# Kernel tuning notes

Hardware: AMD Instinct MI355X
Metric: run time of the kernel (lower is better)

Reference implementation:

```python
import jax, jax.numpy as jnp
import numpy as np
import math

EMBED = 512
KDIM = 512
VDIM = 512
H = 8
HD = EMBED // H
N = 2048
L = 2048
B = 4


def setup_inputs() -> dict:
    key = jax.random.key(0)
    ks = jax.random.split(key, 14)
    s = 1.0 / math.sqrt(EMBED)
    return {
        "q": jax.random.normal(ks[0], (N, B, EMBED), jnp.float32),
        "k": jax.random.normal(ks[1], (L, B, KDIM), jnp.float32),
        "v": jax.random.normal(ks[2], (L, B, VDIM), jnp.float32),
        "pe1": jax.random.normal(ks[3], (B, N, 3), jnp.float32),
        "pe2": jax.random.normal(ks[4], (L, 3), jnp.float32),
        "Wq": jax.random.normal(ks[5], (EMBED, EMBED), jnp.float32) * s,
        "bq": jnp.zeros((EMBED,), jnp.float32),
        "Wk": jax.random.normal(ks[6], (EMBED, KDIM), jnp.float32) * s,
        "bk": jnp.zeros((EMBED,), jnp.float32),
        "Wv": jax.random.normal(ks[7], (EMBED, VDIM), jnp.float32) * s,
        "bv": jnp.zeros((EMBED,), jnp.float32),
        "Wo": jax.random.normal(ks[8], (EMBED, EMBED), jnp.float32) * s,
        "bo": jnp.zeros((EMBED,), jnp.float32),
    }


def reference(q, k, v, pe1, pe2, Wq, bq, Wk, bk, Wv, bv, Wo, bo):
    n, b, _ = q.shape
    l = k.shape[0]
    # projections (nn.Linear: x @ W.T + b)
    qp = q @ Wq.T + bq  # (n, b, E)
    kp = k @ Wk.T + bk  # (l, b, E)
    vp = v @ Wv.T + bv  # (l, b, E)
    # split heads -> (b, H, n, hd)
    qh = qp.reshape(n, b, H, HD).transpose(1, 2, 0, 3)
    kh = kp.reshape(l, b, H, HD).transpose(1, 2, 0, 3)
    vh = vp.reshape(l, b, H, HD).transpose(1, 2, 0, 3)
    # relative PE bias: (b, n, l), broadcast over heads
    pe_scores = jnp.einsum('bnc,lc->bnl', pe1, pe2)[:, None, :, :]
    scores = (jnp.einsum('bhnd,bhld->bhnl', qh, kh) + pe_scores) / math.sqrt(HD)
    attn = jax.nn.softmax(scores, axis=-1)
    out = jnp.einsum('bhnl,bhld->bhnd', attn, vh)  # (b, H, n, hd)
    out = out.transpose(2, 0, 1, 3).reshape(n, b, EMBED)
    return out @ Wo.T + bo
```

## Files before the change

### kernel.cpp

```cpp
#include <hip/hip_runtime.h>
#include <math.h>

#define EMBED 512
#define HDIM 64
#define NHEADS 8
#define SEQ_N 2048
#define SEQ_L 2048
#define BATCH 4
#define MROWS (SEQ_N*BATCH)
#define BE (BATCH*EMBED)

#define QSCALE 0.18033688f

typedef _Float16 f16;
typedef _Float16 half8 __attribute__((ext_vector_type(8)));
typedef _Float16 half4 __attribute__((ext_vector_type(4)));
typedef _Float16 half2v __attribute__((ext_vector_type(2)));
typedef float floatx4 __attribute__((ext_vector_type(4)));
typedef float floatx16 __attribute__((ext_vector_type(16)));

static __device__ inline float fast_exp2(float x) {
#if __has_builtin(__builtin_amdgcn_exp2f)
  return __builtin_amdgcn_exp2f(x);
#else
  return __expf(x * 0.69314718056f);
#endif
}

static __device__ inline half2v pk2(float a, float b) {
#if __has_builtin(__builtin_amdgcn_cvt_pkrtz)
  return __builtin_bit_cast(half2v, __builtin_amdgcn_cvt_pkrtz(a, b));
#else
  half2v o; o[0] = (f16)a; o[1] = (f16)b; return o;
#endif
}

static __device__ inline void gload16(const void* g, void* l) {
  __builtin_amdgcn_global_load_lds(
      (__attribute__((address_space(1))) void*)(g),
      (__attribute__((address_space(3))) void*)(l), 16, 0, 0);
}

__global__ __launch_bounds__(256) void cvt_all(const float* __restrict__ q,
                                               const float* __restrict__ k,
                                               const float* __restrict__ v,
                                               const float* __restrict__ Wq,
                                               const float* __restrict__ Wk,
                                               const float* __restrict__ Wv,
                                               const float* __restrict__ Wo,
                                               f16* __restrict__ qb, f16* __restrict__ kb,
                                               f16* __restrict__ vb, f16* __restrict__ Wb) {
  const long TOK = (long)MROWS * EMBED;
  const long WSZ = (long)EMBED * EMBED;
  int y = blockIdx.y;
  long i = ((long)blockIdx.x * 256 + threadIdx.x) * 4;
  if (y < 3) {
    if (i < TOK) {
      const float* s = y == 0 ? q : y == 1 ? k : v;
      f16* d = y == 0 ? qb : y == 1 ? kb : vb;
      float4 f = *reinterpret_cast<const float4*>(s + i);
      half4 o; o[0] = (f16)f.x; o[1] = (f16)f.y; o[2] = (f16)f.z; o[3] = (f16)f.w;
      *reinterpret_cast<half4*>(d + i) = o;
    }
  } else {
    if (i < 4 * WSZ) {
      int sel = (int)(i >> 18);
      long off = i & (WSZ - 1);
      const float* s = sel == 0 ? Wq : sel == 1 ? Wk : sel == 2 ? Wv : Wo;
      float4 f = *reinterpret_cast<const float4*>(s + off);
      half4 o; o[0] = (f16)f.x; o[1] = (f16)f.y; o[2] = (f16)f.z; o[3] = (f16)f.w;
      *reinterpret_cast<half4*>(Wb + i) = o;
    }
  }
}

__global__ __launch_bounds__(256) void gemm_qkv(const f16* __restrict__ A0,
                                                const f16* __restrict__ A1,
                                                const f16* __restrict__ A2,
                                                const f16* __restrict__ W0,
                                                const f16* __restrict__ W1,
                                                const f16* __restrict__ W2,
                                                const float* __restrict__ b0,
                                                const float* __restrict__ b1,
                                                const float* __restrict__ b2,
                                                f16* __restrict__ C0, f16* __restrict__ C1,
                                                f16* __restrict__ C2) {
  __shared__ alignas(16) f16 As[2][128 * 32];
  __shared__ alignas(16) f16 Bs[2][128 * 32];
  const int sel = blockIdx.y >> 2;
  const f16* A = sel == 0 ? A0 : sel == 1 ? A1 : A2;
  const f16* Bt = sel == 0 ? W0 : sel == 1 ? W1 : W2;
  const float* bias = sel == 0 ? b0 : sel == 1 ? b1 : b2;
  const float scl = sel == 0 ? QSCALE : 1.0f;
  f16* C = sel == 0 ? C0 : sel == 1 ? C1 : C2;
  const int tid = threadIdx.x;
  const int wave = tid >> 6, lane = tid & 63, quad = lane >> 4, l16 = lane & 15;
  const int wm = wave & 1, wn = wave >> 1;
  const long m0 = (long)blockIdx.x * 128;
  const long n0 = (long)(blockIdx.y & 3) * 128;
  const int srow = lane >> 2;
  const int scol = (lane & 3) * 8;

  const f16* Ag0 = A + (m0 + wave * 32 + srow) * EMBED + scol;
  const f16* Ag1 = A + (m0 + wave * 32 + 16 + srow) * EMBED + scol;
  const f16* Bg0 = Bt + (n0 + wave * 32 + srow) * EMBED + scol;
  const f16* Bg1 = Bt + (n0 + wave * 32 + 16 + srow) * EMBED + scol;

  gload16(Ag0, &As[0][(wave * 32) * 32]);
  gload16(Ag1, &As[0][(wave * 32 + 16) * 32]);
  gload16(Bg0, &Bs[0][(wave * 32) * 32]);
  gload16(Bg1, &Bs[0][(wave * 32 + 16) * 32]);
  floatx4 acc[4][4] = {};
  asm volatile("s_waitcnt vmcnt(0)" ::: "memory");
  __builtin_amdgcn_s_barrier();

#pragma unroll
  for (int ks = 0; ks < 16; ++ks) {
    const int cur = ks & 1;
    if (ks + 1 < 16) {
      const int k1 = (ks + 1) * 32;
      gload16(Ag0 + k1, &As[cur ^ 1][(wave * 32) * 32]);
      gload16(Ag1 + k1, &As[cur ^ 1][(wave * 32 + 16) * 32]);
      gload16(Bg0 + k1, &Bs[cur ^ 1][(wave * 32) * 32]);
      gload16(Bg1 + k1, &Bs[cur ^ 1][(wave * 32 + 16) * 32]);
    }
    half8 af[4], bf[4];
#pragma unroll
    for (int i = 0; i < 4; ++i)
      af[i] = *reinterpret_cast<const half8*>(&As[cur][(wm * 64 + i * 16 + l16) * 32 + quad * 8]);
#pragma unroll
    for (int j = 0; j < 4; ++j)
      bf[j] = *reinterpret_cast<const half8*>(&Bs[cur][(wn * 64 + j * 16 + l16) * 32 + quad * 8]);
#pragma unroll
    for (int i = 0; i < 4; ++i)
#pragma unroll
      for (int j = 0; j < 4; ++j)
        acc[i][j] = __builtin_amdgcn_mfma_f32_16x16x32_f16(af[i], bf[j], acc[i][j], 0, 0, 0);
    if (ks + 1 < 16) {
      asm volatile("s_waitcnt vmcnt(0)" ::: "memory");
      __builtin_amdgcn_s_barrier();
    }
  }
#pragma unroll
  for (int i = 0; i < 4; ++i)
#pragma unroll
    for (int r = 0; r < 4; ++r) {
      long row = m0 + wm * 64 + i * 16 + quad * 4 + r;
#pragma unroll
      for (int j = 0; j < 4; ++j) {
        long col = n0 + wn * 64 + j * 16 + l16;
        float val = (acc[i][j][r] + bias[col]) * scl;
        C[row * EMBED + col] = (f16)val;
      }
    }
}

__global__ __launch_bounds__(256) void vtrans(const f16* __restrict__ vp,
                                              f16* __restrict__ vt) {
  __shared__ alignas(16) f16 T[128 * 64];
  const int tid = threadIdx.x;
  const int l0 = blockIdx.x * 128;
  const int bh = blockIdx.y;
  const int b = bh >> 3, h = bh & 7;
  for (int c = tid; c < 1024; c += 256) {
    int r = c >> 3, seg = c & 7;
    uint4 v = *reinterpret_cast<const uint4*>(
        vp + ((long)(l0 + r) * 4 + b) * EMBED + h * 64 + seg * 8);
    int dseg = seg ^ ((r >> 3) & 7);
    *reinterpret_cast<uint4*>(&T[r * 64 + dseg * 8]) = v;
  }
  __syncthreads();
  for (int c = tid; c < 1024; c += 256) {
    int d = c >> 4, seg = c & 15;
    half8 o;
#pragma unroll
    for (int i = 0; i < 8; ++i) {
      int r = seg * 8 + i;
      o[i] = T[r * 64 + (d ^ (((r >> 3) & 7) << 3))];
    }
    *reinterpret_cast<half8*>(vt + ((long)bh * 64 + d) * 2048 + l0 + seg * 8) = o;
  }
}

__global__ __launch_bounds__(256) void gemm_out(const f16* __restrict__ A,
                                                const f16* __restrict__ Bt,
                                                const float* __restrict__ bias,
                                                float* __restrict__ C) {
  __shared__ alignas(16) f16 As[2][128 * 32];
  __shared__ alignas(16) f16 Bs[2][64 * 32];
  const int tid = threadIdx.x;
  const int wave = tid >> 6, lane = tid & 63, quad = lane >> 4, l16 = lane & 15;
  const long m0 = (long)blockIdx.x * 128;
  const long n0 = (long)blockIdx.y * 64;
  const int srow = lane >> 2;
  const int scol = (lane & 3) * 8;

  const f16* Ag0 = A + (m0 + wave * 32 + srow) * EMBED + scol;
  const f16* Ag1 = A + (m0 + wave * 32 + 16 + srow) * EMBED + scol;
  const f16* Bg0 = Bt + (n0 + wave * 16 + srow) * EMBED + scol;

  gload16(Ag0, &As[0][(wave * 32) * 32]);
  gload16(Ag1, &As[0][(wave * 32 + 16) * 32]);
  gload16(Bg0, &Bs[0][(wave * 16) * 32]);
  floatx4 acc[2][4] = {};
  asm volatile("s_waitcnt vmcnt(0)" ::: "memory");
  __builtin_amdgcn_s_barrier();

#pragma unroll
  for (int ks = 0; ks < 16; ++ks) {
    const int cur = ks & 1;
    if (ks + 1 < 16) {
      const int k1 = (ks + 1) * 32;
      gload16(Ag0 + k1, &As[cur ^ 1][(wave * 32) * 32]);
      gload16(Ag1 + k1, &As[cur ^ 1][(wave * 32 + 16) * 32]);
      gload16(Bg0 + k1, &Bs[cur ^ 1][(wave * 16) * 32]);
    }
    half8 af[2], bf[4];
#pragma unroll
    for (int i = 0; i < 2; ++i)
      af[i] = *reinterpret_cast<const half8*>(&As[cur][(wave * 32 + i * 16 + l16) * 32 + quad * 8]);
#pragma unroll
    for (int j = 0; j < 4; ++j)
      bf[j] = *reinterpret_cast<const half8*>(&Bs[cur][(j * 16 + l16) * 32 + quad * 8]);
#pragma unroll
    for (int i = 0; i < 2; ++i)
#pragma unroll
      for (int j = 0; j < 4; ++j)
        acc[i][j] = __builtin_amdgcn_mfma_f32_16x16x32_f16(af[i], bf[j], acc[i][j], 0, 0, 0);
    if (ks + 1 < 16) {
      asm volatile("s_waitcnt vmcnt(0)" ::: "memory");
      __builtin_amdgcn_s_barrier();
    }
  }
#pragma unroll
  for (int i = 0; i < 2; ++i)
#pragma unroll
    for (int r = 0; r < 4; ++r) {
      long row = m0 + wave * 32 + i * 16 + quad * 4 + r;
#pragma unroll
      for (int j = 0; j < 4; ++j) {
        long col = n0 + j * 16 + l16;
        C[row * EMBED + col] = acc[i][j][r] + bias[col];
      }
    }
}

#define KST 88
#define VST 136
#define NCHUNK (SEQ_L / 128)
#define LDSB (128 * KST * 2 + 64 * VST * 2)
__global__ __launch_bounds__(512, 4) void attn_flash(const f16* __restrict__ qp,
                                                     const f16* __restrict__ kp,
                                                     const f16* __restrict__ vt,
                                                     const float* __restrict__ pe1,
                                                     const float* __restrict__ pe2,
                                                     f16* __restrict__ ao) {
  __shared__ alignas(16) unsigned char smem[LDSB];
  f16* Ks = reinterpret_cast<f16*>(smem);
  f16* Vt = reinterpret_cast<f16*>(smem + 128 * KST * 2);
  float* comb = reinterpret_cast<float*>(smem);
  const int tid = threadIdx.x, wave = tid >> 6, lane = tid & 63;
  const int m = lane & 31, h = lane >> 5;
  const int strip = wave & 3, half = wave >> 2;
  const int n0 = blockIdx.x * 128;
  const int b = blockIdx.y >> 3, hd = blockIdx.y & 7;
  const long headoff = (long)b * EMBED + hd * HDIM;
  const long vhead = (long)blockIdx.y * 64 * 2048;

  for (int c = tid; c < 1024; c += 512) {
    int r = c >> 3, col = (c & 7) * 8;
    *reinterpret_cast<uint4*>(&Ks[r * KST + col]) =
        *reinterpret_cast<const uint4*>(qp + (long)(n0 + r) * BE + headoff + col);
    int rv = c >> 4, cv = (c & 15) * 8;
    *reinterpret_cast<uint4*>(&Vt[rv * VST + cv]) =
        *reinterpret_cast<const uint4*>(vt + vhead + (long)rv * 2048 + 0 + cv);
  }
  {
    const uint4 z4 = {0, 0, 0, 0};
    const uint2 z2 = {0, 0};
    int r = tid >> 2, s = tid & 3;
    if (s == 0) *reinterpret_cast<uint2*>(&Ks[r * KST + 68]) = z2;
    else if (s == 1) *reinterpret_cast<uint4*>(&Ks[r * KST + 72]) = z4;
    else if (s == 2) *reinterpret_cast<uint4*>(&Ks[r * KST + 80]) = z4;
  }
  if (tid < 128) {
    long base = ((long)b * SEQ_N + n0 + tid) * 3;
    half4 v8;
    v8[0] = (f16)(pe1[base + 0] * QSCALE);
    v8[1] = (f16)(pe1[base + 1] * QSCALE);
    v8[2] = (f16)(pe1[base + 2] * QSCALE);
    v8[3] = (f16)0.f;
    *reinterpret_cast<half4*>(&Ks[tid * KST + 64]) = v8;
  }
  __syncthreads();

  half8 qf[5];
#pragma unroll
  for (int e = 0; e < 5; ++e)
    qf[e] = *reinterpret_cast<const half8*>(&Ks[(strip * 32 + m) * KST + e * 16 + h * 8]);
  __syncthreads();

  for (int c = tid; c < 1024; c += 512) {
    int r = c >> 3, col = (c & 7) * 8;
    *reinterpret_cast<uint4*>(&Ks[r * KST + col]) =
        *reinterpret_cast<const uint4*>(kp + (long)(0 + r) * BE + headoff + col);
  }
  if (tid < 128) {
    long bb = (long)(0 + tid) * 3;
    half4 p2;
    p2[0] = (f16)pe2[bb + 0]; p2[1] = (f16)pe2[bb + 1];
    p2[2] = (f16)pe2[bb + 2]; p2[3] = (f16)0.f;
    *reinterpret_cast<half4*>(&Ks[tid * KST + 64]) = p2;
  }

  floatx16 oacc[2] = {};
  float lpart = 0.f;

#pragma unroll 1
  for (int c = 0; c < NCHUNK; ++c) {
    __syncthreads();
#pragma unroll
    for (int tt = 0; tt < 2; ++tt) {
      const int t = half * 2 + tt;
      floatx16 st = {};
#pragma unroll
      for (int e = 0; e < 5; ++e) {
        half8 kf = *reinterpret_cast<const half8*>(&Ks[(t * 32 + m) * KST + e * 16 + h * 8]);
        st = __builtin_amdgcn_mfma_f32_32x32x16_f16(kf, qf[e], st, 0, 0, 0);
      }
      float p[16];
#pragma unroll
      for (int r = 0; r < 16; ++r) {
        p[r] = fast_exp2(st[r]);
        lpart += p[r];
      }
#pragma unroll
      for (int s = 0; s < 4; ++s) {
        half2v u0 = pk2(p[4 * s + 0], p[4 * s + 1]);
        half2v u1 = pk2(p[4 * s + 2], p[4 * s + 3]);
        half4 bp;
        bp[0] = u0[0]; bp[1] = u0[1]; bp[2] = u1[0]; bp[3] = u1[1];
        int lcol = t * 32 + s * 8 + h * 4;
#pragma unroll
        for (int dt = 0; dt < 2; ++dt) {
          half4 vf = *reinterpret_cast<const half4*>(&Vt[(dt * 32 + m) * VST + lcol]);
          oacc[dt] = __builtin_amdgcn_mfma_f32_32x32x8f16(vf, bp, oacc[dt], 0, 0, 0);
        }
      }
    }
    __syncthreads();
    if (c + 1 < NCHUNK) {
      const int l0 = (c + 1) * 128;
      for (int cc = tid; cc < 1024; cc += 512) {
        int r = cc >> 3, col = (cc & 7) * 8;
        *reinterpret_cast<uint4*>(&Ks[r * KST + col]) =
            *reinterpret_cast<const uint4*>(kp + (long)(l0 + r) * BE + headoff + col);
        int rv = cc >> 4, cv = (cc & 15) * 8;
        *reinterpret_cast<uint4*>(&Vt[rv * VST + cv]) =
            *reinterpret_cast<const uint4*>(vt + vhead + (long)rv * 2048 + l0 + cv);
      }
      if (tid < 128) {
        long bb = (long)(l0 + tid) * 3;
        half4 p2;
        p2[0] = (f16)pe2[bb + 0]; p2[1] = (f16)pe2[bb + 1];
        p2[2] = (f16)pe2[bb + 2]; p2[3] = (f16)0.f;
        *reinterpret_cast<half4*>(&Ks[tid * KST + 64]) = p2;
      }
    }
  }

  lpart += __shfl_xor(lpart, 32);

  if (half == 1) {
    float* dst = comb + (strip * 64 + lane) * 33;
#pragma unroll
    for (int dt = 0; dt < 2; ++dt)
#pragma unroll
      for (int x = 0; x < 16; ++x) dst[dt * 16 + x] = oacc[dt][x];
    dst[32] = lpart;
  }
  __syncthreads();
  if (half == 0) {
    const float* src = comb + (strip * 64 + lane) * 33;
#pragma unroll
    for (int dt = 0; dt < 2; ++dt)
#pragma unroll
      for (int x = 0; x < 16; ++x) oacc[dt][x] += src[dt * 16 + x];
    float inv = 1.f / (lpart + src[32]);
    long qrow = n0 + strip * 32 + m;
#pragma unroll
    for (int dt = 0; dt < 2; ++dt)
#pragma unroll
      for (int g = 0; g < 4; ++g) {
        half4 o4;
#pragma unroll
        for (int x = 0; x < 4; ++x) o4[x] = (f16)(oacc[dt][4 * g + x] * inv);
        int d = dt * 32 + 8 * g + 4 * h;
        *reinterpret_cast<half4*>(ao + qrow * BE + headoff + d) = o4;
      }
  }
}

extern "C" void kernel_launch(void* const* d_in, const int* in_sizes, int n_in,
                              void* d_out, int out_size, void* d_ws, size_t ws_size,
                              hipStream_t stream) {
  const float* q   = (const float*)d_in[0];
  const float* k   = (const float*)d_in[1];
  const float* v   = (const float*)d_in[2];
  const float* pe1 = (const float*)d_in[3];
  const float* pe2 = (const float*)d_in[4];
  const float* Wq  = (const float*)d_in[5];
  const float* bq  = (const float*)d_in[6];
  const float* Wk  = (const float*)d_in[7];
  const float* bk  = (const float*)d_in[8];
  const float* Wv  = (const float*)d_in[9];
  const float* bv  = (const float*)d_in[10];
  const float* Wo  = (const float*)d_in[11];
  const float* bo  = (const float*)d_in[12];
  float* out = (float*)d_out;

  f16* ws = (f16*)d_ws;
  const long TOK = (long)MROWS * EMBED;
  const long WSZ = (long)EMBED * EMBED;
  f16* qb  = ws;
  f16* kb  = qb + TOK;
  f16* vb  = kb + TOK;
  f16* Wqb = vb + TOK;
  f16* Wkb = Wqb + WSZ;
  f16* Wvb = Wkb + WSZ;
  f16* Wob = Wvb + WSZ;
  f16* qpb = Wob + WSZ;
  f16* kpb = qpb + TOK;
  f16* vtb = kpb + TOK;
  f16* aob = vtb + TOK;
  f16* vpb = aob;

  cvt_all<<<dim3(4096, 4), 256, 0, stream>>>(q, k, v, Wq, Wk, Wv, Wo, qb, kb, vb, Wqb);

  gemm_qkv<<<dim3(MROWS / 128, 12), 256, 0, stream>>>(qb, kb, vb, Wqb, Wkb, Wvb,
                                                      bq, bk, bv, qpb, kpb, vpb);

  vtrans<<<dim3(SEQ_L / 128, BATCH * NHEADS), 256, 0, stream>>>(vpb, vtb);

  attn_flash<<<dim3(SEQ_N / 128, BATCH * NHEADS), 512, 0, stream>>>(qpb, kpb, vtb, pe1, pe2, aob);

  gemm_out<<<dim3(MROWS / 128, EMBED / 64), 256, 0, stream>>>(aob, Wob, bo, out);
}
```

Measured before the change: 210.5 us.

## Fuse V transpose into QKV GEMM epilogue and halve attention query tile

The V projection epilogue now stages results in shared memory and writes V directly in the transposed head-major layout that attention consumes. This removes the separate vtrans kernel and its extra global round trip. Separately, attention blocks now cover 64 query rows instead of 128, with the 8 waves splitting the key chunk four ways. A two-stage shared-memory reduction combines their partial outputs. This doubles the grid for more parallelism, at the cost of reloading K/V tiles twice as often and adding a reduction barrier.

```diff
diff --git a/kernel.cpp b/kernel.cpp
--- a/kernel.cpp
+++ b/kernel.cpp
@@ -84,15 +84,16 @@
                                                 const float* __restrict__ b1,
                                                 const float* __restrict__ b2,
                                                 f16* __restrict__ C0, f16* __restrict__ C1,
-                                                f16* __restrict__ C2) {
-  __shared__ alignas(16) f16 As[2][128 * 32];
-  __shared__ alignas(16) f16 Bs[2][128 * 32];
+                                                f16* __restrict__ C2t) {
+  __shared__ alignas(16) unsigned char gsm[34816];
+  f16* As = reinterpret_cast<f16*>(gsm);
+  f16* Bs = reinterpret_cast<f16*>(gsm + 16384);
+  f16* T  = reinterpret_cast<f16*>(gsm);
   const int sel = blockIdx.y >> 2;
   const f16* A = sel == 0 ? A0 : sel == 1 ? A1 : A2;
   const f16* Bt = sel == 0 ? W0 : sel == 1 ? W1 : W2;
   const float* bias = sel == 0 ? b0 : sel == 1 ? b1 : b2;
   const float scl = sel == 0 ? QSCALE : 1.0f;
-  f16* C = sel == 0 ? C0 : sel == 1 ? C1 : C2;
   const int tid = threadIdx.x;
   const int wave = tid >> 6, lane = tid & 63, quad = lane >> 4, l16 = lane & 15;
   const int wm = wave & 1, wn = wave >> 1;
@@ -106,10 +107,10 @@
   const f16* Bg0 = Bt + (n0 + wave * 32 + srow) * EMBED + scol;
   const f16* Bg1 = Bt + (n0 + wave * 32 + 16 + srow) * EMBED + scol;
 
-  gload16(Ag0, &As[0][(wave * 32) * 32]);
-  gload16(Ag1, &As[0][(wave * 32 + 16) * 32]);
-  gload16(Bg0, &Bs[0][(wave * 32) * 32]);
-  gload16(Bg1, &Bs[0][(wave * 32 + 16) * 32]);
+  gload16(Ag0, &As[(wave * 32) * 32]);
+  gload16(Ag1, &As[(wave * 32 + 16) * 32]);
+  gload16(Bg0, &Bs[(wave * 32) * 32]);
+  gload16(Bg1, &Bs[(wave * 32 + 16) * 32]);
   floatx4 acc[4][4] = {};
   asm volatile("s_waitcnt vmcnt(0)" ::: "memory");
   __builtin_amdgcn_s_barrier();
@@ -119,18 +120,18 @@
     const int cur = ks & 1;
     if (ks + 1 < 16) {
       const int k1 = (ks + 1) * 32;
-      gload16(Ag0 + k1, &As[cur ^ 1][(wave * 32) * 32]);
-      gload16(Ag1 + k1, &As[cur ^ 1][(wave * 32 + 16) * 32]);
-      gload16(Bg0 + k1, &Bs[cur ^ 1][(wave * 32) * 32]);
-      gload16(Bg1 + k1, &Bs[cur ^ 1][(wave * 32 + 16) * 32]);
+      gload16(Ag0 + k1, &As[(cur ^ 1) * 4096 + (wave * 32) * 32]);
+      gload16(Ag1 + k1, &As[(cur ^ 1) * 4096 + (wave * 32 + 16) * 32]);
+      gload16(Bg0 + k1, &Bs[(cur ^ 1) * 4096 + (wave * 32) * 32]);
+      gload16(Bg1 + k1, &Bs[(cur ^ 1) * 4096 + (wave * 32 + 16) * 32]);
     }
     half8 af[4], bf[4];
 #pragma unroll
     for (int i = 0; i < 4; ++i)
-      af[i] = *reinterpret_cast<const half8*>(&As[cur][(wm * 64 + i * 16 + l16) * 32 + quad * 8]);
+      af[i] = *reinterpret_cast<const half8*>(&As[cur * 4096 + (wm * 64 + i * 16 + l16) * 32 + quad * 8]);
 #pragma unroll
     for (int j = 0; j < 4; ++j)
-      bf[j] = *reinterpret_cast<const half8*>(&Bs[cur][(wn * 64 + j * 16 + l16) * 32 + quad * 8]);
+      bf[j] = *reinterpret_cast<const half8*>(&Bs[cur * 4096 + (wn * 64 + j * 16 + l16) * 32 + quad * 8]);
 #pragma unroll
     for (int i = 0; i < 4; ++i)
 #pragma unroll
@@ -141,44 +142,46 @@
       __builtin_amdgcn_s_barrier();
     }
   }
-#pragma unroll
-  for (int i = 0; i < 4; ++i)
-#pragma unroll
-    for (int r = 0; r < 4; ++r) {
-      long row = m0 + wm * 64 + i * 16 + quad * 4 + r;
-#pragma unroll
-      for (int j = 0; j < 4; ++j) {
-        long col = n0 + wn * 64 + j * 16 + l16;
-        float val = (acc[i][j][r] + bias[col]) * scl;
-        C[row * EMBED + col] = (f16)val;
-      }
-    }
-}
-
-__global__ __launch_bounds__(256) void vtrans(const f16* __restrict__ vp,
-                                              f16* __restrict__ vt) {
-  __shared__ alignas(16) f16 T[128 * 64];
-  const int tid = threadIdx.x;
-  const int l0 = blockIdx.x * 128;
-  const int bh = blockIdx.y;
-  const int b = bh >> 3, h = bh & 7;
-  for (int c = tid; c < 1024; c += 256) {
-    int r = c >> 3, seg = c & 7;
-    uint4 v = *reinterpret_cast<const uint4*>(
-        vp + ((long)(l0 + r) * 4 + b) * EMBED + h * 64 + seg * 8);
-    int dseg = seg ^ ((r >> 3) & 7);
-    *reinterpret_cast<uint4*>(&T[r * 64 + dseg * 8]) = v;
-  }
-  __syncthreads();
-  for (int c = tid; c < 1024; c += 256) {
-    int d = c >> 4, seg = c & 15;
-    half8 o;
-#pragma unroll
-    for (int i = 0; i < 8; ++i) {
-      int r = seg * 8 + i;
-      o[i] = T[r * 64 + (d ^ (((r >> 3) & 7) << 3))];
-    }
-    *reinterpret_cast<half8*>(vt + ((long)bh * 64 + d) * 2048 + l0 + seg * 8) = o;
+
+  if (sel != 2) {
+    f16* C = sel == 0 ? C0 : C1;
+#pragma unroll
+    for (int i = 0; i < 4; ++i)
+#pragma unroll
+      for (int r = 0; r < 4; ++r) {
+        long row = m0 + wm * 64 + i * 16 + quad * 4 + r;
+#pragma unroll
+        for (int j = 0; j < 4; ++j) {
+          long col = n0 + wn * 64 + j * 16 + l16;
+          float val = (acc[i][j][r] + bias[col]) * scl;
+          C[row * EMBED + col] = (f16)val;
+        }
+      }
+  } else {
+    __syncthreads();
+#pragma unroll
+    for (int i = 0; i < 4; ++i)
+#pragma unroll
+      for (int r = 0; r < 4; ++r) {
+        int mrow = wm * 64 + i * 16 + quad * 4 + r;
+        int bq = mrow & 3, lt = mrow >> 2;
+#pragma unroll
+        for (int j = 0; j < 4; ++j) {
+          int col = wn * 64 + j * 16 + l16;
+          float val = acc[i][j][r] + bias[n0 + col];
+          T[col * 136 + bq * 32 + lt] = (f16)val;
+        }
+      }
+    __syncthreads();
+    const int h0 = (int)(n0 >> 6);
+    const long lbase = m0 >> 2;
+#pragma unroll
+    for (int it = 0; it < 8; ++it) {
+      int f = it * 256 + tid;
+      int ls = f & 3, bq = (f >> 2) & 3, d6 = (f >> 4) & 63, hl = f >> 10;
+      half8 o = *reinterpret_cast<const half8*>(&T[(hl * 64 + d6) * 136 + bq * 32 + ls * 8]);
+      *reinterpret_cast<half8*>(C2t + (((long)bq * 8 + h0 + hl) * 64 + d6) * 2048 + lbase + ls * 8) = o;
+    }
   }
 }
 
@@ -261,16 +264,19 @@
   float* comb = reinterpret_cast<float*>(smem);
   const int tid = threadIdx.x, wave = tid >> 6, lane = tid & 63;
   const int m = lane & 31, h = lane >> 5;
-  const int strip = wave & 3, half = wave >> 2;
-  const int n0 = blockIdx.x * 128;
+  const int strip = wave & 1;
+  const int half = wave >> 1;
+  const int n0 = blockIdx.x * 64;
   const int b = blockIdx.y >> 3, hd = blockIdx.y & 7;
   const long headoff = (long)b * EMBED + hd * HDIM;
   const long vhead = (long)blockIdx.y * 64 * 2048;
 
-  for (int c = tid; c < 1024; c += 512) {
-    int r = c >> 3, col = (c & 7) * 8;
+  {
+    int r = tid >> 3, col = (tid & 7) * 8;
     *reinterpret_cast<uint4*>(&Ks[r * KST + col]) =
         *reinterpret_cast<const uint4*>(qp + (long)(n0 + r) * BE + headoff + col);
+  }
+  for (int c = tid; c < 1024; c += 512) {
     int rv = c >> 4, cv = (c & 15) * 8;
     *reinterpret_cast<uint4*>(&Vt[rv * VST + cv]) =
         *reinterpret_cast<const uint4*>(vt + vhead + (long)rv * 2048 + 0 + cv);
@@ -283,7 +289,7 @@
     else if (s == 1) *reinterpret_cast<uint4*>(&Ks[r * KST + 72]) = z4;
     else if (s == 2) *reinterpret_cast<uint4*>(&Ks[r * KST + 80]) = z4;
   }
-  if (tid < 128) {
+  if (tid < 64) {
     long base = ((long)b * SEQ_N + n0 + tid) * 3;
     half4 v8;
     v8[0] = (f16)(pe1[base + 0] * QSCALE);
@@ -319,9 +325,8 @@
 #pragma unroll 1
   for (int c = 0; c < NCHUNK; ++c) {
     __syncthreads();
-#pragma unroll
-    for (int tt = 0; tt < 2; ++tt) {
-      const int t = half * 2 + tt;
+    {
+      const int t = half;
       floatx16 st = {};
 #pragma unroll
       for (int e = 0; e < 5; ++e) {
@@ -371,8 +376,8 @@
 
   lpart += __shfl_xor(lpart, 32);
 
-  if (half == 1) {
-    float* dst = comb + (strip * 64 + lane) * 33;
+  if (half & 1) {
+    float* dst = comb + (((strip << 1) + (half >> 1)) * 64 + lane) * 33;
 #pragma unroll
     for (int dt = 0; dt < 2; ++dt)
 #pragma unroll
@@ -380,8 +385,24 @@
     dst[32] = lpart;
   }
   __syncthreads();
+  if (!(half & 1)) {
+    float* slot = comb + (((strip << 1) + (half >> 1)) * 64 + lane) * 33;
+#pragma unroll
+    for (int dt = 0; dt < 2; ++dt)
+#pragma unroll
+      for (int x = 0; x < 16; ++x) oacc[dt][x] += slot[dt * 16 + x];
+    lpart += slot[32];
+    if (half == 2) {
+#pragma unroll
+      for (int dt = 0; dt < 2; ++dt)
+#pragma unroll
+        for (int x = 0; x < 16; ++x) slot[dt * 16 + x] = oacc[dt][x];
+      slot[32] = lpart;
+    }
+  }
+  __syncthreads();
   if (half == 0) {
-    const float* src = comb + (strip * 64 + lane) * 33;
+    const float* src = comb + (((strip << 1) + 1) * 64 + lane) * 33;
 #pragma unroll
     for (int dt = 0; dt < 2; ++dt)
 #pragma unroll
@@ -433,16 +454,13 @@
   f16* kpb = qpb + TOK;
   f16* vtb = kpb + TOK;
   f16* aob = vtb + TOK;
-  f16* vpb = aob;
 
   cvt_all<<<dim3(4096, 4), 256, 0, stream>>>(q, k, v, Wq, Wk, Wv, Wo, qb, kb, vb, Wqb);
 
   gemm_qkv<<<dim3(MROWS / 128, 12), 256, 0, stream>>>(qb, kb, vb, Wqb, Wkb, Wvb,
-                                                      bq, bk, bv, qpb, kpb, vpb);
-
-  vtrans<<<dim3(SEQ_L / 128, BATCH * NHEADS), 256, 0, stream>>>(vpb, vtb);
-
-  attn_flash<<<dim3(SEQ_N / 128, BATCH * NHEADS), 512, 0, stream>>>(qpb, kpb, vtb, pe1, pe2, aob);
+                                                      bq, bk, bv, qpb, kpb, vtb);
+
+  attn_flash<<<dim3(SEQ_N / 64, BATCH * NHEADS), 512, 0, stream>>>(qpb, kpb, vtb, pe1, pe2, aob);
 
   gemm_out<<<dim3(MROWS / 128, EMBED / 64), 256, 0, stream>>>(aob, Wob, bo, out);
 }
```

Measured after the change: 213.1 us. About the same (+1.2%).
